# Kernel optimization log

Hardware: AMD Instinct MI355X
Metric: run time of the kernel (lower is better)

Reference implementation:

```python
import jax, jax.numpy as jnp
import numpy as np

N_NODES = 50000
N_EDGES = 640000
D = 128  # node_dim == edge_dim (required by gate * Vh[dst])
BN_EPS = 1e-5


def _bn(x, gamma, beta):
    # BatchNorm1d in training mode: batch stats over dim 0, biased variance.
    mu = jnp.mean(x, axis=0)
    var = jnp.var(x, axis=0)
    return (x - mu) * jax.lax.rsqrt(var + BN_EPS) * gamma + beta


def setup_inputs() -> dict:
    key = jax.random.key(0)
    ks = jax.random.split(key, 12)
    s = 1.0 / np.sqrt(D)
    h = jax.random.normal(ks[0], (N_NODES, D), dtype=jnp.float32)
    e = jax.random.normal(ks[1], (N_EDGES, D), dtype=jnp.float32)
    edge_index = jax.random.randint(ks[2], (2, N_EDGES), 0, N_NODES)
    mk = lambda k: jax.random.uniform(k, (D, D), jnp.float32, -s, s)
    return {
        "h": h, "e": e, "edge_index": edge_index,
        "Pw": mk(ks[3]), "Qw": mk(ks[4]), "Rw": mk(ks[5]),
        "Uw": mk(ks[6]), "Vw": mk(ks[7]),
        "W1": mk(ks[8]), "b1": jnp.zeros((D,), jnp.float32),
        "W2": mk(ks[9]), "b2": jnp.zeros((D,), jnp.float32),
        "gamma_e": jnp.ones((D,), jnp.float32), "beta_e": jnp.zeros((D,), jnp.float32),
        "gamma_n": jnp.ones((D,), jnp.float32), "beta_n": jnp.zeros((D,), jnp.float32),
        "alpha": jnp.float32(1.0),
    }


def reference(h, e, edge_index, Pw, Qw, Rw, Uw, Vw, W1, b1, W2, b2,
              gamma_e, beta_e, gamma_n, beta_n, alpha):
    src, dst = edge_index[0], edge_index[1]
    # e_hat = P e + Q h[src] + R h[dst]   -> [E, D]
    e_hat = e @ Pw + h[src] @ Qw + h[dst] @ Rw
    # edge update: residual + MLP(BN(e_hat))
    z = _bn(e_hat, gamma_e, beta_e)
    e_new = e + jax.nn.relu(z @ W1 + b1) @ W2 + b2
    # node update: h + alpha * BN(U h + sum_j sigmoid(e_hat) * V h[dst])
    gate = jax.nn.sigmoid(e_hat)
    Vh = h @ Vw
    msg = gate * Vh[dst]                         # [E, D]
    agg = jax.ops.segment_sum(msg, src, num_segments=h.shape[0])
    h_new = h + alpha * _bn(h @ Uw + agg, gamma_n, beta_n)
    return (h_new, e_new)
```

## Files before the change

### kernel.cpp

```cpp
#include <hip/hip_runtime.h>


#define NN 50000
#define NE 640000
#define D 128

typedef unsigned int uint32;
typedef unsigned short u16;
typedef short bf16x8 __attribute__((ext_vector_type(8)));
typedef float floatx4 __attribute__((ext_vector_type(4)));

__device__ __forceinline__ u16 f2bf(float f) {
  uint32 u = __float_as_uint(f);
  u += 0x7fffu + ((u >> 16) & 1u);
  return (u16)(u >> 16);
}
__device__ __forceinline__ float bfu2f(uint32 lo16) { return __uint_as_float(lo16 << 16); }
__device__ __forceinline__ uint32 pack2(float a, float b) {
  return (uint32)f2bf(a) | ((uint32)f2bf(b) << 16);
}
__device__ __forceinline__ float fsigmoid(float x) {
  return __builtin_amdgcn_rcpf(1.f + __expf(-x));
}

__device__ __forceinline__ void mfma_half(const u16* __restrict__ Xs,
                                          const u16* __restrict__ Ws,
                                          floatx4* __restrict__ acc, int wave, int lane) {
  const int q = lane >> 4, l = lane & 15;
  const u16* ax = Xs + (wave * 16 + l) * 136 + q * 8;
  const u16* bx = Ws + l * 136 + q * 8;
#pragma unroll
  for (int kk = 0; kk < 4; ++kk) {
    bf16x8 a = *(const bf16x8*)(ax + kk * 32);
#pragma unroll
    for (int nt = 0; nt < 4; ++nt) {
      bf16x8 b = *(const bf16x8*)(bx + nt * 16 * 136 + kk * 32);
      acc[nt] = __builtin_amdgcn_mfma_f32_16x16x32_bf16(a, b, acc[nt], 0, 0, 0);
    }
  }
}

__device__ __forceinline__ void stage_whalf(u16* __restrict__ Ws, const u16* __restrict__ wsrc,
                                            int tid) {
#pragma unroll
  for (int it = 0; it < 4; ++it) {
    int idx = (it * 256 + tid) * 8;
    *(uint4*)(Ws + (idx >> 7) * 136 + (idx & 127)) = *(const uint4*)(wsrc + idx);
  }
}

__global__ __launch_bounds__(256) void k_wconv(
    const float* __restrict__ Pw, const float* __restrict__ Qw, const float* __restrict__ Rw,
    const float* __restrict__ Uw, const float* __restrict__ Vw, const float* __restrict__ W1,
    const float* __restrict__ W2, u16* __restrict__ wt) {
  int b = blockIdx.x;
  const float* s = (b == 0) ? Pw : (b == 1) ? Qw : (b == 2) ? Rw : (b == 3) ? Uw
                 : (b == 4) ? Vw : (b == 5) ? W1 : W2;
  u16* dstp = wt + b * 16384;
  for (int idx = threadIdx.x; idx < 16384; idx += 256) {
    int k = idx >> 7, n = idx & 127;
    dstp[n * 128 + k] = f2bf(s[idx]);
  }
}

__global__ __launch_bounds__(256, 4) void k_node_gemm(
    const float* __restrict__ h, const u16* __restrict__ wt, float* __restrict__ hQ,
    float* __restrict__ hR, float* __restrict__ hU, float* __restrict__ hV) {
  __shared__ u16 Xs[64 * 136];
  __shared__ u16 Ws[64 * 136];
  const int tid = threadIdx.x;
  const int wave = tid >> 6, lane = tid & 63;
  const int q = lane >> 4, l = lane & 15;
  const int row0 = blockIdx.x * 64;

#pragma unroll
  for (int it = 0; it < 8; ++it) {
    int idx = (it * 256 + tid) * 4;
    int r = idx >> 7, c = idx & 127;
    int g = row0 + r;
    float4 v = make_float4(0.f, 0.f, 0.f, 0.f);
    if (g < NN) v = *(const float4*)(h + (size_t)g * D + c);
    uint2 p;
    p.x = pack2(v.x, v.y);
    p.y = pack2(v.z, v.w);
    *(uint2*)(Xs + r * 136 + c) = p;
  }

  float* const outs[4] = {hQ, hR, hU, hV};
#pragma unroll
  for (int wi = 0; wi < 4; ++wi) {
    __syncthreads();
    stage_whalf(Ws, wt + (wi + 1) * 16384, tid);
    __syncthreads();
    floatx4 acc[8] = {};
    mfma_half(Xs, Ws, acc, wave, lane);
    __syncthreads();
    stage_whalf(Ws, wt + (wi + 1) * 16384 + 8192, tid);
    __syncthreads();
    mfma_half(Xs, Ws, acc + 4, wave, lane);
    float* outp = outs[wi];
#pragma unroll
    for (int nt = 0; nt < 8; ++nt) {
#pragma unroll
      for (int r = 0; r < 4; ++r) {
        int m = wave * 16 + q * 4 + r;
        int g = row0 + m;
        if (g < NN) outp[(size_t)g * D + nt * 16 + l] = acc[nt][r];
      }
    }
  }
}

__global__ __launch_bounds__(256) void k_hist(const int* __restrict__ src,
                                              int* __restrict__ cnt) {
  int i = blockIdx.x * 256 + threadIdx.x;
  if (i < NE) atomicAdd(&cnt[src[i]], 1);
}

__global__ __launch_bounds__(1024) void k_scan(const int* __restrict__ cnt,
                                               int* __restrict__ offs) {
  __shared__ int part[1024];
  const int t = threadIdx.x;
  const int base = t * 49;
  int s = 0;
#pragma unroll 7
  for (int j = 0; j < 49; ++j) {
    int i = base + j;
    if (i < NN) s += cnt[i];
  }
  part[t] = s;
  __syncthreads();
  for (int d = 1; d < 1024; d <<= 1) {
    int v = (t >= d) ? part[t - d] : 0;
    __syncthreads();
    part[t] += v;
    __syncthreads();
  }
  int run = (t == 0) ? 0 : part[t - 1];
  for (int j = 0; j < 49; ++j) {
    int i = base + j;
    if (i < NN) {
      offs[i] = run;
      run += cnt[i];
    }
  }
}

__global__ __launch_bounds__(256) void k_scatter(const int* __restrict__ src,
                                                 const int* __restrict__ dst,
                                                 int* __restrict__ offs,
                                                 int2* __restrict__ sorted) {
  int i = blockIdx.x * 256 + threadIdx.x;
  if (i < NE) {
    int s = src[i];
    int p = atomicAdd(&offs[s], 1);
    sorted[p] = make_int2(i, dst[i]);
  }
}

__global__ __launch_bounds__(256, 4) void k_edge1(
    const float* __restrict__ e, const int* __restrict__ src, const int* __restrict__ dst,
    const u16* __restrict__ wt, const float* __restrict__ hQ, const float* __restrict__ hR,
    u16* __restrict__ ehat, float* __restrict__ esum, float* __restrict__ esq) {
  __shared__ u16 Xs[64 * 136];
  __shared__ u16 Ws[64 * 136];
  __shared__ int sSrc[64], sDst[64];
  __shared__ float sSum[128], sSq[128];
  const int tid = threadIdx.x;
  const int wave = tid >> 6, lane = tid & 63;
  const int q = lane >> 4, l = lane & 15;
  const int row0 = blockIdx.x * 64;

  if (tid < 128) { sSum[tid] = 0.f; sSq[tid] = 0.f; }
  if (tid < 64) { sSrc[tid] = src[row0 + tid]; sDst[tid] = dst[row0 + tid]; }
#pragma unroll
  for (int it = 0; it < 8; ++it) {
    int idx = (it * 256 + tid) * 4;
    int r = idx >> 7, c = idx & 127;
    float4 v = *(const float4*)(e + (size_t)(row0 + r) * D + c);
    uint2 p;
    p.x = pack2(v.x, v.y);
    p.y = pack2(v.z, v.w);
    *(uint2*)(Xs + r * 136 + c) = p;
  }
  stage_whalf(Ws, wt, tid);
  __syncthreads();

  floatx4 acc[8] = {};
  mfma_half(Xs, Ws, acc, wave, lane);
  __syncthreads();
  stage_whalf(Ws, wt + 8192, tid);
  __syncthreads();
  mfma_half(Xs, Ws, acc + 4, wave, lane);

  float cs[8] = {}, cq[8] = {};
#pragma unroll
  for (int nt = 0; nt < 8; ++nt) {
    const int n = nt * 16 + l;
#pragma unroll
    for (int r = 0; r < 4; ++r) {
      const int m = wave * 16 + q * 4 + r;
      const int s = sSrc[m], dd = sDst[m];
      float v = acc[nt][r] + hQ[(size_t)s * D + n] + hR[(size_t)dd * D + n];
      ehat[(size_t)(row0 + m) * D + n] = f2bf(v);
      cs[nt] += v;
      cq[nt] += v * v;
    }
  }
#pragma unroll
  for (int nt = 0; nt < 8; ++nt) {
    cs[nt] += __shfl_xor(cs[nt], 16);
    cs[nt] += __shfl_xor(cs[nt], 32);
    cq[nt] += __shfl_xor(cq[nt], 16);
    cq[nt] += __shfl_xor(cq[nt], 32);
    if (q == 0) {
      atomicAdd(&sSum[nt * 16 + l], cs[nt]);
      atomicAdd(&sSq[nt * 16 + l], cq[nt]);
    }
  }
  __syncthreads();
  if (tid < 128) {
    atomicAdd(&esum[(blockIdx.x & 31) * D + tid], sSum[tid]);
    atomicAdd(&esq[(blockIdx.x & 31) * D + tid], sSq[tid]);
  }
}

__global__ __launch_bounds__(256) void k_agg(
    const u16* __restrict__ ehat, const float* __restrict__ hV, const float* __restrict__ hU,
    const int* __restrict__ cnt, const int* __restrict__ offs, const int2* __restrict__ sorted,
    float* __restrict__ xb, float* __restrict__ nsum, float* __restrict__ nsq) {
  __shared__ float sSum[128], sSq[128];
  const int tid = threadIdx.x;
  if (tid < 128) { sSum[tid] = 0.f; sSq[tid] = 0.f; }
  __syncthreads();
  const int lane = tid & 31;
  const int n = blockIdx.x * 8 + (tid >> 5);
  const int end = offs[n];
  const int deg = cnt[n];
  const int p0 = end - deg;
  const int c4 = lane * 4;
  float4 acc = make_float4(0.f, 0.f, 0.f, 0.f);
  int k = 0;
  for (; k + 4 <= deg; k += 4) {
    int2 ed0 = sorted[p0 + k + 0];
    int2 ed1 = sorted[p0 + k + 1];
    int2 ed2 = sorted[p0 + k + 2];
    int2 ed3 = sorted[p0 + k + 3];
    uint2 ev0 = *(const uint2*)(ehat + (size_t)ed0.x * D + c4);
    uint2 ev1 = *(const uint2*)(ehat + (size_t)ed1.x * D + c4);
    uint2 ev2 = *(const uint2*)(ehat + (size_t)ed2.x * D + c4);
    uint2 ev3 = *(const uint2*)(ehat + (size_t)ed3.x * D + c4);
    float4 v0 = *(const float4*)(hV + (size_t)ed0.y * D + c4);
    float4 v1 = *(const float4*)(hV + (size_t)ed1.y * D + c4);
    float4 v2 = *(const float4*)(hV + (size_t)ed2.y * D + c4);
    float4 v3 = *(const float4*)(hV + (size_t)ed3.y * D + c4);
    acc.x += v0.x * fsigmoid(bfu2f(ev0.x & 0xffffu));
    acc.y += v0.y * fsigmoid(bfu2f(ev0.x >> 16));
    acc.z += v0.z * fsigmoid(bfu2f(ev0.y & 0xffffu));
    acc.w += v0.w * fsigmoid(bfu2f(ev0.y >> 16));
    acc.x += v1.x * fsigmoid(bfu2f(ev1.x & 0xffffu));
    acc.y += v1.y * fsigmoid(bfu2f(ev1.x >> 16));
    acc.z += v1.z * fsigmoid(bfu2f(ev1.y & 0xffffu));
    acc.w += v1.w * fsigmoid(bfu2f(ev1.y >> 16));
    acc.x += v2.x * fsigmoid(bfu2f(ev2.x & 0xffffu));
    acc.y += v2.y * fsigmoid(bfu2f(ev2.x >> 16));
    acc.z += v2.z * fsigmoid(bfu2f(ev2.y & 0xffffu));
    acc.w += v2.w * fsigmoid(bfu2f(ev2.y >> 16));
    acc.x += v3.x * fsigmoid(bfu2f(ev3.x & 0xffffu));
    acc.y += v3.y * fsigmoid(bfu2f(ev3.x >> 16));
    acc.z += v3.z * fsigmoid(bfu2f(ev3.y & 0xffffu));
    acc.w += v3.w * fsigmoid(bfu2f(ev3.y >> 16));
  }
  for (; k < deg; ++k) {
    int2 ed = sorted[p0 + k];
    uint2 ev = *(const uint2*)(ehat + (size_t)ed.x * D + c4);
    float4 v = *(const float4*)(hV + (size_t)ed.y * D + c4);
    acc.x += v.x * fsigmoid(bfu2f(ev.x & 0xffffu));
    acc.y += v.y * fsigmoid(bfu2f(ev.x >> 16));
    acc.z += v.z * fsigmoid(bfu2f(ev.y & 0xffffu));
    acc.w += v.w * fsigmoid(bfu2f(ev.y >> 16));
  }
  float4 u = *(const float4*)(hU + (size_t)n * D + c4);
  float4 x = make_float4(u.x + acc.x, u.y + acc.y, u.z + acc.z, u.w + acc.w);
  *(float4*)(xb + (size_t)n * D + c4) = x;
  atomicAdd(&sSum[c4 + 0], x.x);
  atomicAdd(&sSum[c4 + 1], x.y);
  atomicAdd(&sSum[c4 + 2], x.z);
  atomicAdd(&sSum[c4 + 3], x.w);
  atomicAdd(&sSq[c4 + 0], x.x * x.x);
  atomicAdd(&sSq[c4 + 1], x.y * x.y);
  atomicAdd(&sSq[c4 + 2], x.z * x.z);
  atomicAdd(&sSq[c4 + 3], x.w * x.w);
  __syncthreads();
  if (tid < 128) {
    atomicAdd(&nsum[(blockIdx.x & 31) * D + tid], sSum[tid]);
    atomicAdd(&nsq[(blockIdx.x & 31) * D + tid], sSq[tid]);
  }
}

__global__ __launch_bounds__(128) void k_finalize(
    const float* __restrict__ esum, const float* __restrict__ esq,
    const float* __restrict__ nsum, const float* __restrict__ nsq,
    const float* __restrict__ ge, const float* __restrict__ be, const float* __restrict__ gn,
    const float* __restrict__ bnb, float* __restrict__ sce, float* __restrict__ she,
    float* __restrict__ scn, float* __restrict__ shn) {
  const int t = threadIdx.x;
  float s = 0.f, q = 0.f;
  for (int i = 0; i < 32; ++i) { s += esum[i * D + t]; q += esq[i * D + t]; }
  float mean = s / (float)NE;
  float var = q / (float)NE - mean * mean;
  float istd = rsqrtf(var + 1e-5f);
  sce[t] = istd * ge[t];
  she[t] = be[t] - mean * istd * ge[t];
  s = 0.f; q = 0.f;
  for (int i = 0; i < 32; ++i) { s += nsum[i * D + t]; q += nsq[i * D + t]; }
  mean = s / (float)NN;
  var = q / (float)NN - mean * mean;
  istd = rsqrtf(var + 1e-5f);
  scn[t] = istd * gn[t];
  shn[t] = bnb[t] - mean * istd * gn[t];
}

__global__ __launch_bounds__(256, 4) void k_edge2(
    const u16* __restrict__ ehat, const float* __restrict__ e, const u16* __restrict__ wt,
    const float* __restrict__ sce, const float* __restrict__ she, const float* __restrict__ b1,
    const float* __restrict__ b2, float* __restrict__ oute) {
  __shared__ u16 Ts[64 * 136];
  __shared__ u16 Ws[64 * 136];
  __shared__ float sSc[128], sSh[128], sB1[128], sB2[128];
  const int tid = threadIdx.x;
  const int wave = tid >> 6, lane = tid & 63;
  const int q = lane >> 4, l = lane & 15;
  const int row0 = blockIdx.x * 64;

  if (tid < 128) { sSc[tid] = sce[tid]; sSh[tid] = she[tid]; sB1[tid] = b1[tid]; sB2[tid] = b2[tid]; }
  __syncthreads();

#pragma unroll
  for (int it = 0; it < 4; ++it) {
    int idx = (it * 256 + tid) * 8;
    int r = idx >> 7, c = idx & 127;
    uint4 u = *(const uint4*)(ehat + (size_t)(row0 + r) * D + c);
    float f0 = bfu2f(u.x & 0xffffu) * sSc[c + 0] + sSh[c + 0];
    float f1 = bfu2f(u.x >> 16) * sSc[c + 1] + sSh[c + 1];
    float f2 = bfu2f(u.y & 0xffffu) * sSc[c + 2] + sSh[c + 2];
    float f3 = bfu2f(u.y >> 16) * sSc[c + 3] + sSh[c + 3];
    float f4 = bfu2f(u.z & 0xffffu) * sSc[c + 4] + sSh[c + 4];
    float f5 = bfu2f(u.z >> 16) * sSc[c + 5] + sSh[c + 5];
    float f6 = bfu2f(u.w & 0xffffu) * sSc[c + 6] + sSh[c + 6];
    float f7 = bfu2f(u.w >> 16) * sSc[c + 7] + sSh[c + 7];
    uint4 o;
    o.x = pack2(f0, f1); o.y = pack2(f2, f3); o.z = pack2(f4, f5); o.w = pack2(f6, f7);
    *(uint4*)(Ts + r * 136 + c) = o;
  }
  stage_whalf(Ws, wt + 5 * 16384, tid);
  __syncthreads();

  floatx4 acc[8] = {};
  mfma_half(Ts, Ws, acc, wave, lane);
  __syncthreads();
  stage_whalf(Ws, wt + 5 * 16384 + 8192, tid);
  __syncthreads();
  mfma_half(Ts, Ws, acc + 4, wave, lane);
  __syncthreads();

#pragma unroll
  for (int nt = 0; nt < 8; ++nt) {
    int n = nt * 16 + l;
#pragma unroll
    for (int r = 0; r < 4; ++r) {
      int m = wave * 16 + q * 4 + r;
      float v = acc[nt][r] + sB1[n];
      Ts[m * 136 + n] = f2bf(fmaxf(v, 0.f));
    }
  }
  stage_whalf(Ws, wt + 6 * 16384, tid);
  __syncthreads();

  floatx4 acc2[8] = {};
  mfma_half(Ts, Ws, acc2, wave, lane);
  __syncthreads();
  stage_whalf(Ws, wt + 6 * 16384 + 8192, tid);
  __syncthreads();
  mfma_half(Ts, Ws, acc2 + 4, wave, lane);

#pragma unroll
  for (int nt = 0; nt < 8; ++nt) {
    int n = nt * 16 + l;
#pragma unroll
    for (int r = 0; r < 4; ++r) {
      int m = wave * 16 + q * 4 + r;
      size_t gi = (size_t)(row0 + m) * D + n;
      oute[gi] = e[gi] + acc2[nt][r] + sB2[n];
    }
  }
}

__global__ __launch_bounds__(256) void k_node_out(
    const float* __restrict__ h, const float* __restrict__ xb,
    const float* __restrict__ scn, const float* __restrict__ shn,
    const float* __restrict__ alphap, float* __restrict__ outh) {
  size_t idx = ((size_t)blockIdx.x * 256 + threadIdx.x) * 4;
  int c = (int)(idx & 127);
  float al = alphap[0];
  float4 x = *(const float4*)(xb + idx);
  float4 hh = *(const float4*)(h + idx);
  float4 o;
  o.x = hh.x + al * (x.x * scn[c + 0] + shn[c + 0]);
  o.y = hh.y + al * (x.y * scn[c + 1] + shn[c + 1]);
  o.z = hh.z + al * (x.z * scn[c + 2] + shn[c + 2]);
  o.w = hh.w + al * (x.w * scn[c + 3] + shn[c + 3]);
  *(float4*)(outh + idx) = o;
}

extern "C" void kernel_launch(void* const* d_in, const int* in_sizes, int n_in, void* d_out,
                              int out_size, void* d_ws, size_t ws_size, hipStream_t stream) {
  const float* h = (const float*)d_in[0];
  const float* e = (const float*)d_in[1];
  const int* ei = (const int*)d_in[2];
  const float* Pw = (const float*)d_in[3];
  const float* Qw = (const float*)d_in[4];
  const float* Rw = (const float*)d_in[5];
  const float* Uw = (const float*)d_in[6];
  const float* Vw = (const float*)d_in[7];
  const float* W1 = (const float*)d_in[8];
  const float* b1 = (const float*)d_in[9];
  const float* W2 = (const float*)d_in[10];
  const float* b2 = (const float*)d_in[11];
  const float* ge = (const float*)d_in[12];
  const float* be = (const float*)d_in[13];
  const float* gn = (const float*)d_in[14];
  const float* bnb = (const float*)d_in[15];
  const float* al = (const float*)d_in[16];

  const int* srcp = ei;
  const int* dstp = ei + NE;

  char* ws = (char*)d_ws;
  u16* wt = (u16*)(ws);
  float* hQ = (float*)(ws + 229376ull);
  float* hR = (float*)(ws + 229376ull + 1ull * 25600000ull);
  float* hU = (float*)(ws + 229376ull + 2ull * 25600000ull);
  float* hV = (float*)(ws + 229376ull + 3ull * 25600000ull);
  float* xb = (float*)(ws + 229376ull + 4ull * 25600000ull);
  u16* ehat = (u16*)(ws + 229376ull + 5ull * 25600000ull);
  char* statb = ws + 229376ull + 5ull * 25600000ull + 163840000ull;
  float* esum = (float*)(statb);
  float* esq = (float*)(statb + 16384);
  float* nsum = (float*)(statb + 32768);
  float* nsq = (float*)(statb + 49152);
  float* sce = (float*)(statb + 65536);
  float* she = (float*)(statb + 65536 + 512);
  float* scn = (float*)(statb + 65536 + 1024);
  float* shn = (float*)(statb + 65536 + 1536);
  char* sortb = statb + 67584;
  int* cnt = (int*)(sortb);
  int* offs = (int*)(sortb + 200704);
  int2* sorted = (int2*)(sortb + 401408);

  float* outh = (float*)d_out;
  float* oute = outh + (size_t)NN * D;

  hipMemsetAsync(statb, 0, 67584 + 200704, stream);

  k_wconv<<<7, 256, 0, stream>>>(Pw, Qw, Rw, Uw, Vw, W1, W2, wt);
  k_hist<<<2500, 256, 0, stream>>>(srcp, cnt);
  k_scan<<<1, 1024, 0, stream>>>(cnt, offs);
  k_scatter<<<2500, 256, 0, stream>>>(srcp, dstp, offs, sorted);
  k_node_gemm<<<782, 256, 0, stream>>>(h, wt, hQ, hR, hU, hV);
  k_edge1<<<10000, 256, 0, stream>>>(e, srcp, dstp, wt, hQ, hR, ehat, esum, esq);
  k_agg<<<6250, 256, 0, stream>>>(ehat, hV, hU, cnt, offs, sorted, xb, nsum, nsq);
  k_finalize<<<1, 128, 0, stream>>>(esum, esq, nsum, nsq, ge, be, gn, bnb, sce, she, scn, shn);
  k_edge2<<<10000, 256, 0, stream>>>(ehat, e, wt, sce, she, b1, b2, oute);
  k_node_out<<<6250, 256, 0, stream>>>(h, xb, scn, shn, al, outh);
}
```

Baseline: 1.137 ms.

## Process edges in src-sorted order and fold edge BN into W1

Edge kernels now walk edges in source-sorted order. The edge features are gathered by edge id and e_hat is written in sorted order, so aggregation reads e_hat contiguously instead of gathering it, and hQ reads gain locality. The edge BatchNorm scale and shift are folded into a transposed bf16 copy of W1 plus an adjusted bias inside the finalize kernel, which removes the per-element normalize pass in edge2. The cost is that the e loads in edge1 and the e/oute accesses in edge2 become row gathers and scatters, and the single-block finalize now does a 128x128 weight transform.

Result: slower. 1.161 ms (+2.1%).

```diff
diff --git a/kernel.cpp b/kernel.cpp
--- a/kernel.cpp
+++ b/kernel.cpp
@@ -149,19 +149,24 @@
 __global__ __launch_bounds__(256) void k_scatter(const int* __restrict__ src,
                                                  const int* __restrict__ dst,
                                                  int* __restrict__ offs,
-                                                 int2* __restrict__ sorted) {
+                                                 int* __restrict__ eidS,
+                                                 int* __restrict__ srcS,
+                                                 int* __restrict__ dstS) {
   int i = blockIdx.x * 256 + threadIdx.x;
   if (i < NE) {
-    int s = src[i];
+    int s = src[i], d = dst[i];
     int p = atomicAdd(&offs[s], 1);
-    sorted[p] = make_int2(i, dst[i]);
+    eidS[p] = i;
+    srcS[p] = s;
+    dstS[p] = d;
   }
 }
 
 __global__ __launch_bounds__(256, 4) void k_edge1(
-    const float* __restrict__ e, const int* __restrict__ src, const int* __restrict__ dst,
-    const u16* __restrict__ wt, const float* __restrict__ hQ, const float* __restrict__ hR,
-    u16* __restrict__ ehat, float* __restrict__ esum, float* __restrict__ esq) {
+    const float* __restrict__ e, const int* __restrict__ eidS, const int* __restrict__ srcS,
+    const int* __restrict__ dstS, const u16* __restrict__ wt, const float* __restrict__ hQ,
+    const float* __restrict__ hR, u16* __restrict__ ehat_s, float* __restrict__ esum,
+    float* __restrict__ esq) {
   __shared__ u16 Xs[64 * 136];
   __shared__ u16 Ws[64 * 136];
   __shared__ int sSrc[64], sDst[64];
@@ -172,12 +177,13 @@
   const int row0 = blockIdx.x * 64;
 
   if (tid < 128) { sSum[tid] = 0.f; sSq[tid] = 0.f; }
-  if (tid < 64) { sSrc[tid] = src[row0 + tid]; sDst[tid] = dst[row0 + tid]; }
+  if (tid < 64) { sSrc[tid] = srcS[row0 + tid]; sDst[tid] = dstS[row0 + tid]; }
 #pragma unroll
   for (int it = 0; it < 8; ++it) {
     int idx = (it * 256 + tid) * 4;
     int r = idx >> 7, c = idx & 127;
-    float4 v = *(const float4*)(e + (size_t)(row0 + r) * D + c);
+    int eid = eidS[row0 + r];
+    float4 v = *(const float4*)(e + (size_t)eid * D + c);
     uint2 p;
     p.x = pack2(v.x, v.y);
     p.y = pack2(v.z, v.w);
@@ -202,7 +208,7 @@
       const int m = wave * 16 + q * 4 + r;
       const int s = sSrc[m], dd = sDst[m];
       float v = acc[nt][r] + hQ[(size_t)s * D + n] + hR[(size_t)dd * D + n];
-      ehat[(size_t)(row0 + m) * D + n] = f2bf(v);
+      ehat_s[(size_t)(row0 + m) * D + n] = f2bf(v);
       cs[nt] += v;
       cq[nt] += v * v;
     }
@@ -226,8 +232,8 @@
 }
 
 __global__ __launch_bounds__(256) void k_agg(
-    const u16* __restrict__ ehat, const float* __restrict__ hV, const float* __restrict__ hU,
-    const int* __restrict__ cnt, const int* __restrict__ offs, const int2* __restrict__ sorted,
+    const u16* __restrict__ ehat_s, const float* __restrict__ hV, const float* __restrict__ hU,
+    const int* __restrict__ cnt, const int* __restrict__ offs, const int* __restrict__ dstS,
     float* __restrict__ xb, float* __restrict__ nsum, float* __restrict__ nsq) {
   __shared__ float sSum[128], sSq[128];
   const int tid = threadIdx.x;
@@ -242,18 +248,18 @@
   float4 acc = make_float4(0.f, 0.f, 0.f, 0.f);
   int k = 0;
   for (; k + 4 <= deg; k += 4) {
-    int2 ed0 = sorted[p0 + k + 0];
-    int2 ed1 = sorted[p0 + k + 1];
-    int2 ed2 = sorted[p0 + k + 2];
-    int2 ed3 = sorted[p0 + k + 3];
-    uint2 ev0 = *(const uint2*)(ehat + (size_t)ed0.x * D + c4);
-    uint2 ev1 = *(const uint2*)(ehat + (size_t)ed1.x * D + c4);
-    uint2 ev2 = *(const uint2*)(ehat + (size_t)ed2.x * D + c4);
-    uint2 ev3 = *(const uint2*)(ehat + (size_t)ed3.x * D + c4);
-    float4 v0 = *(const float4*)(hV + (size_t)ed0.y * D + c4);
-    float4 v1 = *(const float4*)(hV + (size_t)ed1.y * D + c4);
-    float4 v2 = *(const float4*)(hV + (size_t)ed2.y * D + c4);
-    float4 v3 = *(const float4*)(hV + (size_t)ed3.y * D + c4);
+    int d0 = dstS[p0 + k + 0];
+    int d1 = dstS[p0 + k + 1];
+    int d2 = dstS[p0 + k + 2];
+    int d3 = dstS[p0 + k + 3];
+    uint2 ev0 = *(const uint2*)(ehat_s + (size_t)(p0 + k + 0) * D + c4);
+    uint2 ev1 = *(const uint2*)(ehat_s + (size_t)(p0 + k + 1) * D + c4);
+    uint2 ev2 = *(const uint2*)(ehat_s + (size_t)(p0 + k + 2) * D + c4);
+    uint2 ev3 = *(const uint2*)(ehat_s + (size_t)(p0 + k + 3) * D + c4);
+    float4 v0 = *(const float4*)(hV + (size_t)d0 * D + c4);
+    float4 v1 = *(const float4*)(hV + (size_t)d1 * D + c4);
+    float4 v2 = *(const float4*)(hV + (size_t)d2 * D + c4);
+    float4 v3 = *(const float4*)(hV + (size_t)d3 * D + c4);
     acc.x += v0.x * fsigmoid(bfu2f(ev0.x & 0xffffu));
     acc.y += v0.y * fsigmoid(bfu2f(ev0.x >> 16));
     acc.z += v0.z * fsigmoid(bfu2f(ev0.y & 0xffffu));
@@ -272,9 +278,9 @@
     acc.w += v3.w * fsigmoid(bfu2f(ev3.y >> 16));
   }
   for (; k < deg; ++k) {
-    int2 ed = sorted[p0 + k];
-    uint2 ev = *(const uint2*)(ehat + (size_t)ed.x * D + c4);
-    float4 v = *(const float4*)(hV + (size_t)ed.y * D + c4);
+    int dd = dstS[p0 + k];
+    uint2 ev = *(const uint2*)(ehat_s + (size_t)(p0 + k) * D + c4);
+    float4 v = *(const float4*)(hV + (size_t)dd * D + c4);
     acc.x += v.x * fsigmoid(bfu2f(ev.x & 0xffffu));
     acc.y += v.y * fsigmoid(bfu2f(ev.x >> 16));
     acc.z += v.z * fsigmoid(bfu2f(ev.y & 0xffffu));
@@ -302,16 +308,20 @@
     const float* __restrict__ esum, const float* __restrict__ esq,
     const float* __restrict__ nsum, const float* __restrict__ nsq,
     const float* __restrict__ ge, const float* __restrict__ be, const float* __restrict__ gn,
-    const float* __restrict__ bnb, float* __restrict__ sce, float* __restrict__ she,
-    float* __restrict__ scn, float* __restrict__ shn) {
+    const float* __restrict__ bnb, const float* __restrict__ W1, const float* __restrict__ b1,
+    float* __restrict__ scn, float* __restrict__ shn, u16* __restrict__ wt7,
+    float* __restrict__ b1p) {
+  __shared__ float sSc[128], sSh[128];
   const int t = threadIdx.x;
   float s = 0.f, q = 0.f;
   for (int i = 0; i < 32; ++i) { s += esum[i * D + t]; q += esq[i * D + t]; }
   float mean = s / (float)NE;
   float var = q / (float)NE - mean * mean;
   float istd = rsqrtf(var + 1e-5f);
-  sce[t] = istd * ge[t];
-  she[t] = be[t] - mean * istd * ge[t];
+  float sce = istd * ge[t];
+  float she = be[t] - mean * sce;
+  sSc[t] = sce;
+  sSh[t] = she;
   s = 0.f; q = 0.f;
   for (int i = 0; i < 32; ++i) { s += nsum[i * D + t]; q += nsq[i * D + t]; }
   mean = s / (float)NN;
@@ -319,47 +329,45 @@
   istd = rsqrtf(var + 1e-5f);
   scn[t] = istd * gn[t];
   shn[t] = bnb[t] - mean * istd * gn[t];
+  __syncthreads();
+  float acc = b1[t];
+  for (int k = 0; k < 128; ++k) {
+    float w = W1[k * D + t];
+    acc += sSh[k] * w;
+    wt7[t * D + k] = f2bf(sSc[k] * w);
+  }
+  b1p[t] = acc;
 }
 
 __global__ __launch_bounds__(256, 4) void k_edge2(
-    const u16* __restrict__ ehat, const float* __restrict__ e, const u16* __restrict__ wt,
-    const float* __restrict__ sce, const float* __restrict__ she, const float* __restrict__ b1,
-    const float* __restrict__ b2, float* __restrict__ oute) {
+    const u16* __restrict__ ehat_s, const int* __restrict__ eidS, const float* __restrict__ e,
+    const u16* __restrict__ wt, const float* __restrict__ b1p, const float* __restrict__ b2,
+    float* __restrict__ oute) {
   __shared__ u16 Ts[64 * 136];
   __shared__ u16 Ws[64 * 136];
-  __shared__ float sSc[128], sSh[128], sB1[128], sB2[128];
+  __shared__ float sB1[128], sB2[128];
+  __shared__ int sEid[64];
   const int tid = threadIdx.x;
   const int wave = tid >> 6, lane = tid & 63;
   const int q = lane >> 4, l = lane & 15;
   const int row0 = blockIdx.x * 64;
 
-  if (tid < 128) { sSc[tid] = sce[tid]; sSh[tid] = she[tid]; sB1[tid] = b1[tid]; sB2[tid] = b2[tid]; }
-  __syncthreads();
+  if (tid < 128) { sB1[tid] = b1p[tid]; sB2[tid] = b2[tid]; }
+  if (tid < 64) sEid[tid] = eidS[row0 + tid];
 
 #pragma unroll
   for (int it = 0; it < 4; ++it) {
     int idx = (it * 256 + tid) * 8;
     int r = idx >> 7, c = idx & 127;
-    uint4 u = *(const uint4*)(ehat + (size_t)(row0 + r) * D + c);
-    float f0 = bfu2f(u.x & 0xffffu) * sSc[c + 0] + sSh[c + 0];
-    float f1 = bfu2f(u.x >> 16) * sSc[c + 1] + sSh[c + 1];
-    float f2 = bfu2f(u.y & 0xffffu) * sSc[c + 2] + sSh[c + 2];
-    float f3 = bfu2f(u.y >> 16) * sSc[c + 3] + sSh[c + 3];
-    float f4 = bfu2f(u.z & 0xffffu) * sSc[c + 4] + sSh[c + 4];
-    float f5 = bfu2f(u.z >> 16) * sSc[c + 5] + sSh[c + 5];
-    float f6 = bfu2f(u.w & 0xffffu) * sSc[c + 6] + sSh[c + 6];
-    float f7 = bfu2f(u.w >> 16) * sSc[c + 7] + sSh[c + 7];
-    uint4 o;
-    o.x = pack2(f0, f1); o.y = pack2(f2, f3); o.z = pack2(f4, f5); o.w = pack2(f6, f7);
-    *(uint4*)(Ts + r * 136 + c) = o;
-  }
-  stage_whalf(Ws, wt + 5 * 16384, tid);
+    *(uint4*)(Ts + r * 136 + c) = *(const uint4*)(ehat_s + (size_t)(row0 + r) * D + c);
+  }
+  stage_whalf(Ws, wt + 7 * 16384, tid);
   __syncthreads();
 
   floatx4 acc[8] = {};
   mfma_half(Ts, Ws, acc, wave, lane);
   __syncthreads();
-  stage_whalf(Ws, wt + 5 * 16384 + 8192, tid);
+  stage_whalf(Ws, wt + 7 * 16384 + 8192, tid);
   __syncthreads();
   mfma_half(Ts, Ws, acc + 4, wave, lane);
   __syncthreads();
@@ -390,7 +398,7 @@
 #pragma unroll
     for (int r = 0; r < 4; ++r) {
       int m = wave * 16 + q * 4 + r;
-      size_t gi = (size_t)(row0 + m) * D + n;
+      size_t gi = (size_t)sEid[m] * D + n;
       oute[gi] = e[gi] + acc2[nt][r] + sB2[n];
     }
   }
@@ -438,39 +446,41 @@
 
   char* ws = (char*)d_ws;
   u16* wt = (u16*)(ws);
-  float* hQ = (float*)(ws + 229376ull);
-  float* hR = (float*)(ws + 229376ull + 1ull * 25600000ull);
-  float* hU = (float*)(ws + 229376ull + 2ull * 25600000ull);
-  float* hV = (float*)(ws + 229376ull + 3ull * 25600000ull);
-  float* xb = (float*)(ws + 229376ull + 4ull * 25600000ull);
-  u16* ehat = (u16*)(ws + 229376ull + 5ull * 25600000ull);
-  char* statb = ws + 229376ull + 5ull * 25600000ull + 163840000ull;
+  float* hQ = (float*)(ws + 262144ull);
+  float* hR = (float*)(ws + 262144ull + 1ull * 25600000ull);
+  float* hU = (float*)(ws + 262144ull + 2ull * 25600000ull);
+  float* hV = (float*)(ws + 262144ull + 3ull * 25600000ull);
+  float* xb = (float*)(ws + 262144ull + 4ull * 25600000ull);
+  u16* ehat = (u16*)(ws + 128262144ull);
+  char* statb = ws + 292102144ull;
   float* esum = (float*)(statb);
   float* esq = (float*)(statb + 16384);
   float* nsum = (float*)(statb + 32768);
   float* nsq = (float*)(statb + 49152);
-  float* sce = (float*)(statb + 65536);
-  float* she = (float*)(statb + 65536 + 512);
-  float* scn = (float*)(statb + 65536 + 1024);
-  float* shn = (float*)(statb + 65536 + 1536);
-  char* sortb = statb + 67584;
+  float* scn = (float*)(statb + 65536);
+  float* shn = (float*)(statb + 66048);
+  float* b1p = (float*)(statb + 66560);
+  char* sortb = ws + 292171776ull;
   int* cnt = (int*)(sortb);
   int* offs = (int*)(sortb + 200704);
-  int2* sorted = (int2*)(sortb + 401408);
+  int* eidS = (int*)(sortb + 401408);
+  int* srcS = (int*)(sortb + 2961408);
+  int* dstS = (int*)(sortb + 5521408);
 
   float* outh = (float*)d_out;
   float* oute = outh + (size_t)NN * D;
 
-  hipMemsetAsync(statb, 0, 67584 + 200704, stream);
+  hipMemsetAsync(statb, 0, 69632 + 200704, stream);
 
   k_wconv<<<7, 256, 0, stream>>>(Pw, Qw, Rw, Uw, Vw, W1, W2, wt);
   k_hist<<<2500, 256, 0, stream>>>(srcp, cnt);
   k_scan<<<1, 1024, 0, stream>>>(cnt, offs);
-  k_scatter<<<2500, 256, 0, stream>>>(srcp, dstp, offs, sorted);
+  k_scatter<<<2500, 256, 0, stream>>>(srcp, dstp, offs, eidS, srcS, dstS);
   k_node_gemm<<<782, 256, 0, stream>>>(h, wt, hQ, hR, hU, hV);
-  k_edge1<<<10000, 256, 0, stream>>>(e, srcp, dstp, wt, hQ, hR, ehat, esum, esq);
-  k_agg<<<6250, 256, 0, stream>>>(ehat, hV, hU, cnt, offs, sorted, xb, nsum, nsq);
-  k_finalize<<<1, 128, 0, stream>>>(esum, esq, nsum, nsq, ge, be, gn, bnb, sce, she, scn, shn);
-  k_edge2<<<10000, 256, 0, stream>>>(ehat, e, wt, sce, she, b1, b2, oute);
+  k_edge1<<<10000, 256, 0, stream>>>(e, eidS, srcS, dstS, wt, hQ, hR, ehat, esum, esq);
+  k_agg<<<6250, 256, 0, stream>>>(ehat, hV, hU, cnt, offs, dstS, xb, nsum, nsq);
+  k_finalize<<<1, 128, 0, stream>>>(esum, esq, nsum, nsq, ge, be, gn, bnb, W1, b1,
+                                    scn, shn, wt + 7 * 16384, b1p);
+  k_edge2<<<10000, 256, 0, stream>>>(ehat, eidS, e, wt, b1p, b2, oute);
   k_node_out<<<6250, 256, 0, stream>>>(h, xb, scn, shn, al, outh);
 }
```
